# Optimization experiments

Measured on AMD Instinct MI355X. Metric: run time of the kernel, lower is better.

## Reference

```python
import jax, jax.numpy as jnp
import numpy as np

# LE-like radial basis config (hypers: type='le', r_cut=5.0, mlp=True, no alchemical)
N_MAX_L = [22, 19, 16, 13]      # n_max per angular channel l
L_MAX = len(N_MAX_L) - 1
N_TOTAL = sum(N_MAX_L)          # 70
N_SPECIES = 4                   # all_species = [0,1,2,3]
N_GRID = 1024                   # spline control points
R_CUT = 5.0
HIDDEN = 32                     # hard-coded MLP width in the module
N_EDGES = 400_000


def setup_inputs() -> dict:
    key = jax.random.key(0)
    ks = jax.random.split(key, 7)
    # neighbor distances in [0, r_cut)
    r = jax.random.uniform(ks[0], (N_EDGES,), dtype=jnp.float32) * R_CUT
    neighbor_species = jax.random.randint(ks[1], (N_EDGES,), 0, N_SPECIES)
    # spline table standing in for the precomputed spliner coefficients
    spline_table = jax.random.normal(ks[2], (N_GRID, N_TOTAL), dtype=jnp.float32)
    nmax = max(N_MAX_L)
    sc_in = 1.0 / np.sqrt(nmax)
    sc_h = 1.0 / np.sqrt(HIDDEN)
    # per-(l, species) expert MLP weights, padded to nmax along the n_max_l axis;
    # torch Linear(n_in, n_out, bias=False) == x @ W with W: [n_in, n_out]
    W1 = jax.random.normal(ks[3], (L_MAX + 1, N_SPECIES, nmax, HIDDEN), dtype=jnp.float32) * sc_in
    W2 = jax.random.normal(ks[4], (L_MAX + 1, N_SPECIES, HIDDEN, HIDDEN), dtype=jnp.float32) * sc_h
    W3 = jax.random.normal(ks[5], (L_MAX + 1, N_SPECIES, HIDDEN, HIDDEN), dtype=jnp.float32) * sc_h
    W4 = jax.random.normal(ks[6], (L_MAX + 1, N_SPECIES, HIDDEN, nmax), dtype=jnp.float32) * sc_h
    return {"r": r, "neighbor_species": neighbor_species, "spline_table": spline_table,
            "W1": W1, "W2": W2, "W3": W3, "W4": W4}


def _spline_eval(r, spline_table):
    # linear-interpolation spline over a uniform grid on [0, R_CUT]
    dx = R_CUT / (N_GRID - 1)
    xi = r / dx
    idx = jnp.clip(jnp.floor(xi).astype(jnp.int32), 0, N_GRID - 2)
    frac = (xi - idx.astype(xi.dtype))[:, None]
    return spline_table[idx] * (1.0 - frac) + spline_table[idx + 1] * frac  # [E, N_TOTAL]


def reference(r, neighbor_species, spline_table, W1, W2, W3, W4):
    # 1) spline basis eval: r -> radial_functions [E, N_TOTAL]
    rf = _spline_eval(r, spline_table)
    silu = jax.nn.silu
    outs = []
    off = 0
    # 2) split by n_max_l; per-species expert MLP with scatter-back.
    # Vectorized as: run each species' tiny MLP on all edges, select via mask
    # (equivalent math to the original's nonzero/index_select gather-scatter).
    for l, n_l in enumerate(N_MAX_L):
        x_l = rf[:, off:off + n_l]  # [E, n_l]
        off += n_l
        out_l = jnp.zeros_like(x_l)
        for s in range(N_SPECIES):
            h = silu(x_l @ W1[l, s, :n_l])        # [E, 32]
            h = silu(h @ W2[l, s])                # [E, 32]
            h = silu(h @ W3[l, s])                # [E, 32]
            y = h @ W4[l, s][:, :n_l]             # [E, n_l]
            out_l = jnp.where(neighbor_species[:, None] == s, y, out_l)
        outs.append(out_l)
    # original returns a list split by l; concatenate for a single output array
    return jnp.concatenate(outs, axis=1)  # [E, N_TOTAL]
```

## Files before the change

### kernel.cpp

```cpp
#include <hip/hip_runtime.h>
#include <math.h>

#define BLK 256
#define BX 192
#define NEDGE_MAX 400000
#define TSL 24608

typedef __attribute__((ext_vector_type(8))) short short8;
typedef __attribute__((ext_vector_type(4))) float f32x4;

union Frag {
  short8 s;
  unsigned int u[4];
};

__device__ __forceinline__ unsigned int pack_pair(float a, float b) {
  const unsigned int ua = __float_as_uint(a) + 0x8000u;
  const unsigned int ub = __float_as_uint(b) + 0x8000u;
  return (ua >> 16) | (ub & 0xFFFF0000u);
}

__device__ __forceinline__ void split_pair(float a, float b, unsigned int& hi,
                                           unsigned int& lo) {
  hi = pack_pair(a, b);
  const float ra = a - __uint_as_float(hi << 16);
  const float rb = b - __uint_as_float(hi & 0xFFFF0000u);
  lo = pack_pair(ra, rb);
}

__device__ __forceinline__ f32x4 silu4(f32x4 v) {
#pragma unroll
  for (int i = 0; i < 4; i++) {
    const float e = __builtin_amdgcn_exp2f(v[i] * -1.44269504f);
    v[i] = v[i] * __builtin_amdgcn_rcpf(1.0f + e);
  }
  return v;
}


__global__ void k_zero(int* __restrict__ cnt) {
  if (threadIdx.x < 4) cnt[threadIdx.x] = 0;
}

__global__ void __launch_bounds__(BLK) k_compact(const int* __restrict__ spc,
                                                 const float* __restrict__ r, int n,
                                                 int nb, int* __restrict__ cnt,
                                                 float* __restrict__ fracs,
                                                 int* __restrict__ toffA,
                                                 int* __restrict__ perm,
                                                 const float* __restrict__ tbl,
                                                 float* __restrict__ wt) {
  if (blockIdx.x >= nb) {
    const int t = (blockIdx.x - nb) * BLK + threadIdx.x;
    if (t < 4 * 1024 * 24) {
      const int l = t / (1024 * 24);
      const int rem = t - l * (1024 * 24);
      const int idx = rem / 24;
      const int j = rem - idx * 24;
      const int off = (l == 0) ? 0 : (l == 1) ? 22 : (l == 2) ? 41 : 57;
      const int nl = (l == 0) ? 22 : (l == 1) ? 19 : (l == 2) ? 16 : 13;
      const float v = (j < nl) ? tbl[idx * 70 + off + j] : 0.f;
      wt[l * TSL + idx * 24 + j] = v;
    }
    if (t < 4 * 32) {
      const int l = t >> 5, j = t & 31;
      wt[l * TSL + 1024 * 24 + j] = 0.f;
    }
    return;
  }

  __shared__ int wcnt[4][4];
  __shared__ int wbase[4][4];
  const int tid = threadIdx.x;
  const int i = blockIdx.x * BLK + tid;
  const int lane = tid & 63;
  const int w = tid >> 6;
  const int s = (i < n) ? spc[i] : -1;
  const float rr = (i < n) ? r[i] : 0.f;

  int rank = 0;
#pragma unroll
  for (int sp = 0; sp < 4; sp++) {
    unsigned long long m = __ballot(s == sp);
    if (lane == 0) wcnt[w][sp] = __popcll(m);
    if (s == sp) rank = __popcll(m & ((1ULL << lane) - 1ULL));
  }
  __syncthreads();
  if (tid < 4) {
    const int c0 = wcnt[0][tid], c1 = wcnt[1][tid], c2 = wcnt[2][tid], c3 = wcnt[3][tid];
    const int b = atomicAdd(&cnt[tid], c0 + c1 + c2 + c3);
    wbase[0][tid] = b;
    wbase[1][tid] = b + c0;
    wbase[2][tid] = b + c0 + c1;
    wbase[3][tid] = b + c0 + c1 + c2;
  }
  __syncthreads();
  if (s >= 0) {
    const int pos = s * NEDGE_MAX + wbase[w][s] + rank;
    const float xi = rr * (1023.0f / 5.0f);
    int idx = (int)floorf(xi);
    idx = idx < 0 ? 0 : (idx > 1022 ? 1022 : idx);
    fracs[pos] = xi - (float)idx;
    toffA[pos] = idx * 96;
    perm[pos] = i;
  }
}


__device__ __forceinline__ void layer_hl(const Frag* A, const Frag& bh,
                                         const Frag& bl, f32x4& d0, f32x4& d1) {
  f32x4 z = {0.f, 0.f, 0.f, 0.f};
  d0 = __builtin_amdgcn_mfma_f32_16x16x32_bf16(A[0].s, bl.s, z, 0, 0, 0);
  d0 = __builtin_amdgcn_mfma_f32_16x16x32_bf16(A[0].s, bh.s, d0, 0, 0, 0);
  d1 = __builtin_amdgcn_mfma_f32_16x16x32_bf16(A[1].s, bl.s, z, 0, 0, 0);
  d1 = __builtin_amdgcn_mfma_f32_16x16x32_bf16(A[1].s, bh.s, d1, 0, 0, 0);
}

__device__ __forceinline__ void layer_h(const Frag* A, const Frag& bh, f32x4& d0,
                                        f32x4& d1) {
  f32x4 z = {0.f, 0.f, 0.f, 0.f};
  d0 = __builtin_amdgcn_mfma_f32_16x16x32_bf16(A[0].s, bh.s, z, 0, 0, 0);
  d1 = __builtin_amdgcn_mfma_f32_16x16x32_bf16(A[1].s, bh.s, z, 0, 0, 0);
}

__device__ __forceinline__ void ldA(const unsigned int* __restrict__ wfr,
                                    int base256, int lane, Frag* A) {
#pragma unroll
  for (int jt = 0; jt < 2; jt++) {
    const uint4 v =
        reinterpret_cast<const uint4*>(wfr + ((base256 + jt) << 8))[lane];
    A[jt].u[0] = v.x;
    A[jt].u[1] = v.y;
    A[jt].u[2] = v.z;
    A[jt].u[3] = v.w;
  }
}

__device__ __forceinline__ void repack(const f32x4& d0, const f32x4& d1,
                                       Frag& bh) {
  bh.u[0] = pack_pair(d0[0], d0[1]);
  bh.u[1] = pack_pair(d0[2], d0[3]);
  bh.u[2] = pack_pair(d1[0], d1[1]);
  bh.u[3] = pack_pair(d1[2], d1[3]);
}

template <int L, int UBASE, int G1>
__device__ __forceinline__ void proc_l(const unsigned int* __restrict__ wfr,
                                       const float* __restrict__ wt, int toff,
                                       float frac, int g, int lane,
                                       unsigned int* __restrict__ xrow) {
  const char* p = (const char*)(wt + (size_t)L * TSL + 8 * g) + toff;
  const f32x4 a0 = *(const f32x4*)(p);
  const f32x4 a1 = *(const f32x4*)(p + 16);
  const f32x4 b0 = *(const f32x4*)(p + 96);
  const f32x4 b1 = *(const f32x4*)(p + 112);

  Frag A1[2], A2[2], A3[2], A4[2];
  ldA(wfr, (L * 4 + 0) * 2, lane, A1);
  ldA(wfr, (L * 4 + 1) * 2, lane, A2);
  ldA(wfr, (L * 4 + 2) * 2, lane, A3);
  ldA(wfr, (L * 4 + 3) * 2, lane, A4);

  float x[8];
#pragma unroll
  for (int d = 0; d < 4; d++) {
    x[d] = a0[d] + frac * (b0[d] - a0[d]);
    x[d + 4] = a1[d] + frac * (b1[d] - a1[d]);
  }
  Frag bh, bl;
  split_pair(x[0], x[1], bh.u[0], bl.u[0]);
  split_pair(x[2], x[3], bh.u[1], bl.u[1]);
  split_pair(x[4], x[5], bh.u[2], bl.u[2]);
  split_pair(x[6], x[7], bh.u[3], bl.u[3]);

  f32x4 d0, d1;
  layer_hl(A1, bh, bl, d0, d1);
  d0 = silu4(d0); d1 = silu4(d1); repack(d0, d1, bh);
  layer_h(A2, bh, d0, d1);
  d0 = silu4(d0); d1 = silu4(d1); repack(d0, d1, bh);
  layer_h(A3, bh, d0, d1);
  d0 = silu4(d0); d1 = silu4(d1); repack(d0, d1, bh);
  f32x4 z = {0.f, 0.f, 0.f, 0.f};
  d0 = __builtin_amdgcn_mfma_f32_16x16x32_bf16(A4[0].s, bh.s, z, 0, 0, 0);
  if (G1 > 0) d1 = __builtin_amdgcn_mfma_f32_16x16x32_bf16(A4[1].s, bh.s, z, 0, 0, 0);

  *(uint2*)(xrow + UBASE + 2 * g) =
      make_uint2(pack_pair(d0[0], d0[1]), pack_pair(d0[2], d0[3]));
  if (G1 > 0 && g < G1)
    *(uint2*)(xrow + UBASE + 8 + 2 * g) =
        make_uint2(pack_pair(d1[0], d1[1]), pack_pair(d1[2], d1[3]));
}

__global__ void __launch_bounds__(BLK) rb_fused(
    const float* __restrict__ fracs, const int* __restrict__ toffA,
    const int* __restrict__ perm, const float* __restrict__ wt,
    const float* __restrict__ W1, const float* __restrict__ W2,
    const float* __restrict__ W3, const float* __restrict__ W4,
    float* __restrict__ out, const int* __restrict__ cnt) {
  __shared__ unsigned int wfr[8192];
  __shared__ unsigned int xp[4][16 * 38];
  __shared__ int eid[4][16];

  const int s = blockIdx.y;
  const int count = cnt[s];
  if (count == 0) return;
  const int sBase = s * NEDGE_MAX;

  {
    const int nlarr[4] = {22, 19, 16, 13};
    for (int e = threadIdx.x; e < 8192; e += BLK) {
      const int p = e & 3;
      const int lane = (e >> 2) & 63;
      const int jt = (e >> 8) & 1;
      const int m = (e >> 9) & 3;
      const int l = e >> 11;
      const int c = lane & 15, g = lane >> 4;
      const int j = jt * 16 + c;
      const int nl = nlarr[l];
      float a, b;
      if (m == 0) {
        const int k0 = 8 * g + 2 * p, k1 = k0 + 1;
        const float* wp = W1 + (size_t)(l * 4 + s) * 704;
        a = (k0 < nl) ? wp[k0 * 32 + j] : 0.f;
        b = (k1 < nl) ? wp[k1 * 32 + j] : 0.f;
      } else {
        const int kp0 = (p < 2) ? (4 * g + 2 * p) : (16 + 4 * g + 2 * (p - 2));
        const int kp1 = kp0 + 1;
        if (m == 1) {
          const float* wp = W2 + (size_t)(l * 4 + s) * 1024;
          a = wp[kp0 * 32 + j];
          b = wp[kp1 * 32 + j];
        } else if (m == 2) {
          const float* wp = W3 + (size_t)(l * 4 + s) * 1024;
          a = wp[kp0 * 32 + j];
          b = wp[kp1 * 32 + j];
        } else {
          const float* wp = W4 + (size_t)(l * 4 + s) * 704;
          a = (j < nl) ? wp[kp0 * 22 + j] : 0.f;
          b = (j < nl) ? wp[kp1 * 22 + j] : 0.f;
        }
      }
      wfr[e] = pack_pair(a, b);
    }
  }
  __syncthreads();

  const int lane = threadIdx.x & 63;
  const int w = threadIdx.x >> 6;
  const int c = lane & 15, g = lane >> 4;
  unsigned int* __restrict__ xpw = xp[w];
  int* __restrict__ eidw = eid[w];
  unsigned int* __restrict__ xrow = xpw + c * 38;
  const int stride = gridDim.x * 64;

  int eb = blockIdx.x * 64 + w * 16;
  int valid = (eb + c) < count;
  int spi = sBase + (valid ? eb + c : 0);
  float frac = fracs[spi];
  int toff = toffA[spi];
  int e0 = perm[spi];

  for (; eb < count; eb += stride) {
    const int nei = eb + stride + c;
    const int nvalid = nei < count;
    const int nspi = sBase + (nvalid ? nei : 0);
    const float nfrac = fracs[nspi];
    const int ntoff = toffA[nspi];
    const int ne = perm[nspi];

    proc_l<0, 0, 2>(wfr, wt, toff, frac, g, lane, xrow);
    proc_l<1, 12, 1>(wfr, wt, toff, frac, g, lane, xrow);
    proc_l<2, 22, 0>(wfr, wt, toff, frac, g, lane, xrow);
    proc_l<3, 30, 0>(wfr, wt, toff, frac, g, lane, xrow);

    if (g == 0) eidw[c] = valid ? e0 : -1;
    __asm__ volatile("" ::: "memory");

#pragma unroll
    for (int it = 0; it < 18; it++) {
      const int t = it * 64 + lane;
      if (t < 16 * 70) {
        const int row = t / 70;
        const int f = t - row * 70;
        const int er = eidw[row];
        const int fl = f + ((f >= 22) ? 2 : 0) + ((f >= 41) ? 1 : 0);
        const unsigned int v = xpw[row * 38 + (fl >> 1)];
        const unsigned int hv = (fl & 1) ? (v & 0xFFFF0000u) : (v << 16);
        if (er >= 0) out[(size_t)er * 70 + f] = __uint_as_float(hv);
      }
    }
    __asm__ volatile("" ::: "memory");

    frac = nfrac;
    toff = ntoff;
    e0 = ne;
    valid = nvalid;
  }
}

extern "C" void kernel_launch(void* const* d_in, const int* in_sizes, int n_in,
                              void* d_out, int out_size, void* d_ws, size_t ws_size,
                              hipStream_t stream) {
  const float* r = (const float*)d_in[0];
  const int* spc = (const int*)d_in[1];
  const float* tbl = (const float*)d_in[2];
  const float* W1 = (const float*)d_in[3];
  const float* W2 = (const float*)d_in[4];
  const float* W3 = (const float*)d_in[5];
  const float* W4 = (const float*)d_in[6];
  float* out = (float*)d_out;
  const int n = in_sizes[0];

  int* cnt = (int*)d_ws;
  float* fracs = (float*)(cnt + 64);
  int* toffA = (int*)(fracs + 4 * NEDGE_MAX);
  int* perm = toffA + 4 * NEDGE_MAX;
  float* wtbl = (float*)(perm + 4 * NEDGE_MAX);

  hipLaunchKernelGGL(k_zero, dim3(1), dim3(64), 0, stream, cnt);

  const int nb = (n + BLK - 1) / BLK;
  hipLaunchKernelGGL(k_compact, dim3(nb + 384), dim3(BLK), 0, stream, spc, r, n,
                     nb, cnt, fracs, toffA, perm, tbl, wtbl);

  hipLaunchKernelGGL(rb_fused, dim3(BX, 4), dim3(BLK), 0, stream, fracs, toffA,
                     perm, wtbl, W1, W2, W3, W4, out, cnt);
}
```

Before: 123.1 us.

## Pre-pack MLP weight fragments in global memory and drop LDS weight staging

Moves the per-species bf16 weight-fragment packing out of the main kernel into extra blocks of the compaction kernel, writing fragments to a global workspace. The main kernel then reads weight fragments straight from global/L2 with software prefetch, one layer ahead, instead of staging 32KB in LDS per block. It also stores outputs as fp32 in LDS rather than truncated bf16, and raises the grid width with an occupancy hint of 5 blocks per CU. Freeing LDS should allow more resident blocks and removes the per-block packing prologue, at the cost of repeated global fragment loads per edge tile.

Result: slower. 251.5 us (+104.4%).

```diff
diff --git a/kernel.cpp b/kernel.cpp
--- a/kernel.cpp
+++ b/kernel.cpp
@@ -2,7 +2,7 @@
 #include <math.h>
 
 #define BLK 256
-#define BX 192
+#define BX 320
 #define NEDGE_MAX 400000
 #define TSL 24608
 
@@ -49,166 +49,34 @@
                                                  int* __restrict__ toffA,
                                                  int* __restrict__ perm,
                                                  const float* __restrict__ tbl,
-                                                 float* __restrict__ wt) {
+                                                 float* __restrict__ wt,
+                                                 unsigned int* __restrict__ wg,
+                                                 const float* __restrict__ W1,
+                                                 const float* __restrict__ W2,
+                                                 const float* __restrict__ W3,
+                                                 const float* __restrict__ W4) {
   if (blockIdx.x >= nb) {
-    const int t = (blockIdx.x - nb) * BLK + threadIdx.x;
-    if (t < 4 * 1024 * 24) {
-      const int l = t / (1024 * 24);
-      const int rem = t - l * (1024 * 24);
-      const int idx = rem / 24;
-      const int j = rem - idx * 24;
-      const int off = (l == 0) ? 0 : (l == 1) ? 22 : (l == 2) ? 41 : 57;
-      const int nl = (l == 0) ? 22 : (l == 1) ? 19 : (l == 2) ? 16 : 13;
-      const float v = (j < nl) ? tbl[idx * 70 + off + j] : 0.f;
-      wt[l * TSL + idx * 24 + j] = v;
-    }
-    if (t < 4 * 32) {
-      const int l = t >> 5, j = t & 31;
-      wt[l * TSL + 1024 * 24 + j] = 0.f;
-    }
-    return;
-  }
-
-  __shared__ int wcnt[4][4];
-  __shared__ int wbase[4][4];
-  const int tid = threadIdx.x;
-  const int i = blockIdx.x * BLK + tid;
-  const int lane = tid & 63;
-  const int w = tid >> 6;
-  const int s = (i < n) ? spc[i] : -1;
-  const float rr = (i < n) ? r[i] : 0.f;
-
-  int rank = 0;
-#pragma unroll
-  for (int sp = 0; sp < 4; sp++) {
-    unsigned long long m = __ballot(s == sp);
-    if (lane == 0) wcnt[w][sp] = __popcll(m);
-    if (s == sp) rank = __popcll(m & ((1ULL << lane) - 1ULL));
-  }
-  __syncthreads();
-  if (tid < 4) {
-    const int c0 = wcnt[0][tid], c1 = wcnt[1][tid], c2 = wcnt[2][tid], c3 = wcnt[3][tid];
-    const int b = atomicAdd(&cnt[tid], c0 + c1 + c2 + c3);
-    wbase[0][tid] = b;
-    wbase[1][tid] = b + c0;
-    wbase[2][tid] = b + c0 + c1;
-    wbase[3][tid] = b + c0 + c1 + c2;
-  }
-  __syncthreads();
-  if (s >= 0) {
-    const int pos = s * NEDGE_MAX + wbase[w][s] + rank;
-    const float xi = rr * (1023.0f / 5.0f);
-    int idx = (int)floorf(xi);
-    idx = idx < 0 ? 0 : (idx > 1022 ? 1022 : idx);
-    fracs[pos] = xi - (float)idx;
-    toffA[pos] = idx * 96;
-    perm[pos] = i;
-  }
-}
-
-
-__device__ __forceinline__ void layer_hl(const Frag* A, const Frag& bh,
-                                         const Frag& bl, f32x4& d0, f32x4& d1) {
-  f32x4 z = {0.f, 0.f, 0.f, 0.f};
-  d0 = __builtin_amdgcn_mfma_f32_16x16x32_bf16(A[0].s, bl.s, z, 0, 0, 0);
-  d0 = __builtin_amdgcn_mfma_f32_16x16x32_bf16(A[0].s, bh.s, d0, 0, 0, 0);
-  d1 = __builtin_amdgcn_mfma_f32_16x16x32_bf16(A[1].s, bl.s, z, 0, 0, 0);
-  d1 = __builtin_amdgcn_mfma_f32_16x16x32_bf16(A[1].s, bh.s, d1, 0, 0, 0);
-}
-
-__device__ __forceinline__ void layer_h(const Frag* A, const Frag& bh, f32x4& d0,
-                                        f32x4& d1) {
-  f32x4 z = {0.f, 0.f, 0.f, 0.f};
-  d0 = __builtin_amdgcn_mfma_f32_16x16x32_bf16(A[0].s, bh.s, z, 0, 0, 0);
-  d1 = __builtin_amdgcn_mfma_f32_16x16x32_bf16(A[1].s, bh.s, z, 0, 0, 0);
-}
-
-__device__ __forceinline__ void ldA(const unsigned int* __restrict__ wfr,
-                                    int base256, int lane, Frag* A) {
-#pragma unroll
-  for (int jt = 0; jt < 2; jt++) {
-    const uint4 v =
-        reinterpret_cast<const uint4*>(wfr + ((base256 + jt) << 8))[lane];
-    A[jt].u[0] = v.x;
-    A[jt].u[1] = v.y;
-    A[jt].u[2] = v.z;
-    A[jt].u[3] = v.w;
-  }
-}
-
-__device__ __forceinline__ void repack(const f32x4& d0, const f32x4& d1,
-                                       Frag& bh) {
-  bh.u[0] = pack_pair(d0[0], d0[1]);
-  bh.u[1] = pack_pair(d0[2], d0[3]);
-  bh.u[2] = pack_pair(d1[0], d1[1]);
-  bh.u[3] = pack_pair(d1[2], d1[3]);
-}
-
-template <int L, int UBASE, int G1>
-__device__ __forceinline__ void proc_l(const unsigned int* __restrict__ wfr,
-                                       const float* __restrict__ wt, int toff,
-                                       float frac, int g, int lane,
-                                       unsigned int* __restrict__ xrow) {
-  const char* p = (const char*)(wt + (size_t)L * TSL + 8 * g) + toff;
-  const f32x4 a0 = *(const f32x4*)(p);
-  const f32x4 a1 = *(const f32x4*)(p + 16);
-  const f32x4 b0 = *(const f32x4*)(p + 96);
-  const f32x4 b1 = *(const f32x4*)(p + 112);
-
-  Frag A1[2], A2[2], A3[2], A4[2];
-  ldA(wfr, (L * 4 + 0) * 2, lane, A1);
-  ldA(wfr, (L * 4 + 1) * 2, lane, A2);
-  ldA(wfr, (L * 4 + 2) * 2, lane, A3);
-  ldA(wfr, (L * 4 + 3) * 2, lane, A4);
-
-  float x[8];
-#pragma unroll
-  for (int d = 0; d < 4; d++) {
-    x[d] = a0[d] + frac * (b0[d] - a0[d]);
-    x[d + 4] = a1[d] + frac * (b1[d] - a1[d]);
-  }
-  Frag bh, bl;
-  split_pair(x[0], x[1], bh.u[0], bl.u[0]);
-  split_pair(x[2], x[3], bh.u[1], bl.u[1]);
-  split_pair(x[4], x[5], bh.u[2], bl.u[2]);
-  split_pair(x[6], x[7], bh.u[3], bl.u[3]);
-
-  f32x4 d0, d1;
-  layer_hl(A1, bh, bl, d0, d1);
-  d0 = silu4(d0); d1 = silu4(d1); repack(d0, d1, bh);
-  layer_h(A2, bh, d0, d1);
-  d0 = silu4(d0); d1 = silu4(d1); repack(d0, d1, bh);
-  layer_h(A3, bh, d0, d1);
-  d0 = silu4(d0); d1 = silu4(d1); repack(d0, d1, bh);
-  f32x4 z = {0.f, 0.f, 0.f, 0.f};
-  d0 = __builtin_amdgcn_mfma_f32_16x16x32_bf16(A4[0].s, bh.s, z, 0, 0, 0);
-  if (G1 > 0) d1 = __builtin_amdgcn_mfma_f32_16x16x32_bf16(A4[1].s, bh.s, z, 0, 0, 0);
-
-  *(uint2*)(xrow + UBASE + 2 * g) =
-      make_uint2(pack_pair(d0[0], d0[1]), pack_pair(d0[2], d0[3]));
-  if (G1 > 0 && g < G1)
-    *(uint2*)(xrow + UBASE + 8 + 2 * g) =
-        make_uint2(pack_pair(d1[0], d1[1]), pack_pair(d1[2], d1[3]));
-}
-
-__global__ void __launch_bounds__(BLK) rb_fused(
-    const float* __restrict__ fracs, const int* __restrict__ toffA,
-    const int* __restrict__ perm, const float* __restrict__ wt,
-    const float* __restrict__ W1, const float* __restrict__ W2,
-    const float* __restrict__ W3, const float* __restrict__ W4,
-    float* __restrict__ out, const int* __restrict__ cnt) {
-  __shared__ unsigned int wfr[8192];
-  __shared__ unsigned int xp[4][16 * 38];
-  __shared__ int eid[4][16];
-
-  const int s = blockIdx.y;
-  const int count = cnt[s];
-  if (count == 0) return;
-  const int sBase = s * NEDGE_MAX;
-
-  {
-    const int nlarr[4] = {22, 19, 16, 13};
-    for (int e = threadIdx.x; e < 8192; e += BLK) {
+    const int reg2 = blockIdx.x - nb;
+    if (reg2 < 384) {
+      const int t = reg2 * BLK + threadIdx.x;
+      if (t < 4 * 1024 * 24) {
+        const int l = t / (1024 * 24);
+        const int rem = t - l * (1024 * 24);
+        const int idx = rem / 24;
+        const int j = rem - idx * 24;
+        const int off = (l == 0) ? 0 : (l == 1) ? 22 : (l == 2) ? 41 : 57;
+        const int nl = (l == 0) ? 22 : (l == 1) ? 19 : (l == 2) ? 16 : 13;
+        const float v = (j < nl) ? tbl[idx * 70 + off + j] : 0.f;
+        wt[l * TSL + idx * 24 + j] = v;
+      }
+      if (t < 4 * 32) {
+        const int l = t >> 5, j = t & 31;
+        wt[l * TSL + 1024 * 24 + j] = 0.f;
+      }
+    } else {
+      const int eg = (reg2 - 384) * BLK + threadIdx.x;
+      const int s = eg >> 13;
+      const int e = eg & 8191;
       const int p = e & 3;
       const int lane = (e >> 2) & 63;
       const int jt = (e >> 8) & 1;
@@ -216,7 +84,7 @@
       const int l = e >> 11;
       const int c = lane & 15, g = lane >> 4;
       const int j = jt * 16 + c;
-      const int nl = nlarr[l];
+      const int nl = (l == 0) ? 22 : (l == 1) ? 19 : (l == 2) ? 16 : 13;
       float a, b;
       if (m == 0) {
         const int k0 = 8 * g + 2 * p, k1 = k0 + 1;
@@ -240,17 +108,153 @@
           b = (j < nl) ? wp[kp1 * 22 + j] : 0.f;
         }
       }
-      wfr[e] = pack_pair(a, b);
+      wg[eg] = pack_pair(a, b);
     }
+    return;
+  }
+
+  __shared__ int wcnt[4][4];
+  __shared__ int wbase[4][4];
+  const int tid = threadIdx.x;
+  const int i = blockIdx.x * BLK + tid;
+  const int lane = tid & 63;
+  const int w = tid >> 6;
+  const int s = (i < n) ? spc[i] : -1;
+  const float rr = (i < n) ? r[i] : 0.f;
+
+  int rank = 0;
+#pragma unroll
+  for (int sp = 0; sp < 4; sp++) {
+    unsigned long long m = __ballot(s == sp);
+    if (lane == 0) wcnt[w][sp] = __popcll(m);
+    if (s == sp) rank = __popcll(m & ((1ULL << lane) - 1ULL));
   }
   __syncthreads();
+  if (tid < 4) {
+    const int c0 = wcnt[0][tid], c1 = wcnt[1][tid], c2 = wcnt[2][tid], c3 = wcnt[3][tid];
+    const int b = atomicAdd(&cnt[tid], c0 + c1 + c2 + c3);
+    wbase[0][tid] = b;
+    wbase[1][tid] = b + c0;
+    wbase[2][tid] = b + c0 + c1;
+    wbase[3][tid] = b + c0 + c1 + c2;
+  }
+  __syncthreads();
+  if (s >= 0) {
+    const int pos = s * NEDGE_MAX + wbase[w][s] + rank;
+    const float xi = rr * (1023.0f / 5.0f);
+    int idx = (int)floorf(xi);
+    idx = idx < 0 ? 0 : (idx > 1022 ? 1022 : idx);
+    fracs[pos] = xi - (float)idx;
+    toffA[pos] = idx * 96;
+    perm[pos] = i;
+  }
+}
+
+
+__device__ __forceinline__ void layer_hl(const Frag* A, const Frag& bh,
+                                         const Frag& bl, f32x4& d0, f32x4& d1) {
+  f32x4 z = {0.f, 0.f, 0.f, 0.f};
+  d0 = __builtin_amdgcn_mfma_f32_16x16x32_bf16(A[0].s, bl.s, z, 0, 0, 0);
+  d0 = __builtin_amdgcn_mfma_f32_16x16x32_bf16(A[0].s, bh.s, d0, 0, 0, 0);
+  d1 = __builtin_amdgcn_mfma_f32_16x16x32_bf16(A[1].s, bl.s, z, 0, 0, 0);
+  d1 = __builtin_amdgcn_mfma_f32_16x16x32_bf16(A[1].s, bh.s, d1, 0, 0, 0);
+}
+
+__device__ __forceinline__ void layer_h(const Frag* A, const Frag& bh, f32x4& d0,
+                                        f32x4& d1) {
+  f32x4 z = {0.f, 0.f, 0.f, 0.f};
+  d0 = __builtin_amdgcn_mfma_f32_16x16x32_bf16(A[0].s, bh.s, z, 0, 0, 0);
+  d1 = __builtin_amdgcn_mfma_f32_16x16x32_bf16(A[1].s, bh.s, z, 0, 0, 0);
+}
+
+__device__ __forceinline__ void ldG(const unsigned int* __restrict__ wgs,
+                                    int base256, int lane, Frag* A) {
+#pragma unroll
+  for (int jt = 0; jt < 2; jt++) {
+    const uint4 v =
+        reinterpret_cast<const uint4*>(wgs + ((base256 + jt) << 8))[lane];
+    A[jt].u[0] = v.x;
+    A[jt].u[1] = v.y;
+    A[jt].u[2] = v.z;
+    A[jt].u[3] = v.w;
+  }
+}
+
+__device__ __forceinline__ void repack(const f32x4& d0, const f32x4& d1,
+                                       Frag& bh) {
+  bh.u[0] = pack_pair(d0[0], d0[1]);
+  bh.u[1] = pack_pair(d0[2], d0[3]);
+  bh.u[2] = pack_pair(d1[0], d1[1]);
+  bh.u[3] = pack_pair(d1[2], d1[3]);
+}
+
+template <int L>
+__device__ __forceinline__ void gather_split(const float* __restrict__ wt,
+                                             int toff, float frac, int g,
+                                             Frag& bh, Frag& bl) {
+  const char* p = (const char*)(wt + (size_t)L * TSL + 8 * g) + toff;
+  const f32x4 a0 = *(const f32x4*)(p);
+  const f32x4 a1 = *(const f32x4*)(p + 16);
+  const f32x4 b0 = *(const f32x4*)(p + 96);
+  const f32x4 b1 = *(const f32x4*)(p + 112);
+  float x[8];
+#pragma unroll
+  for (int d = 0; d < 4; d++) {
+    x[d] = a0[d] + frac * (b0[d] - a0[d]);
+    x[d + 4] = a1[d] + frac * (b1[d] - a1[d]);
+  }
+  split_pair(x[0], x[1], bh.u[0], bl.u[0]);
+  split_pair(x[2], x[3], bh.u[1], bl.u[1]);
+  split_pair(x[4], x[5], bh.u[2], bl.u[2]);
+  split_pair(x[6], x[7], bh.u[3], bl.u[3]);
+}
+
+template <int L, int OFFA, int G1>
+__device__ __forceinline__ void proc_l(const unsigned int* __restrict__ wgs,
+                                       const float* __restrict__ wt, int toff,
+                                       float frac, int g, int lane,
+                                       float* __restrict__ xrow) {
+  Frag Aa[2], Ab[2];
+  ldG(wgs, (L * 4 + 0) * 2, lane, Aa);
+  Frag bh, bl;
+  gather_split<L>(wt, toff, frac, g, bh, bl);
+  ldG(wgs, (L * 4 + 1) * 2, lane, Ab);
+  f32x4 d0, d1;
+  layer_hl(Aa, bh, bl, d0, d1);
+  d0 = silu4(d0); d1 = silu4(d1); repack(d0, d1, bh);
+  ldG(wgs, (L * 4 + 2) * 2, lane, Aa);
+  layer_h(Ab, bh, d0, d1);
+  d0 = silu4(d0); d1 = silu4(d1); repack(d0, d1, bh);
+  ldG(wgs, (L * 4 + 3) * 2, lane, Ab);
+  layer_h(Aa, bh, d0, d1);
+  d0 = silu4(d0); d1 = silu4(d1); repack(d0, d1, bh);
+  f32x4 z = {0.f, 0.f, 0.f, 0.f};
+  d0 = __builtin_amdgcn_mfma_f32_16x16x32_bf16(Ab[0].s, bh.s, z, 0, 0, 0);
+  if (G1 > 0) d1 = __builtin_amdgcn_mfma_f32_16x16x32_bf16(Ab[1].s, bh.s, z, 0, 0, 0);
+  *(f32x4*)(xrow + OFFA + 4 * g) = d0;
+  if (G1 > 0 && g < G1) *(f32x4*)(xrow + OFFA + 16 + 4 * g) = d1;
+}
+
+__global__ void __launch_bounds__(BLK, 5) rb_fused(
+    const float* __restrict__ fracs, const int* __restrict__ toffA,
+    const int* __restrict__ perm, const float* __restrict__ wt,
+    const unsigned int* __restrict__ wg, float* __restrict__ out,
+    const int* __restrict__ cnt) {
+  __shared__ float xp[4][16 * 76];
+  __shared__ int eid[4][16];
+
+  const int s = blockIdx.y;
+  const int count = cnt[s];
+  if (count == 0) return;
+  const int sBase = s * NEDGE_MAX;
+  const unsigned int* __restrict__ wgs = wg + s * 8192;
 
   const int lane = threadIdx.x & 63;
   const int w = threadIdx.x >> 6;
   const int c = lane & 15, g = lane >> 4;
-  unsigned int* __restrict__ xpw = xp[w];
+  float* __restrict__ xpw = xp[w];
   int* __restrict__ eidw = eid[w];
-  unsigned int* __restrict__ xrow = xpw + c * 38;
+  float* __restrict__ xrow = xpw + c * 76;
   const int stride = gridDim.x * 64;
 
   int eb = blockIdx.x * 64 + w * 16;
@@ -268,10 +272,10 @@
     const int ntoff = toffA[nspi];
     const int ne = perm[nspi];
 
-    proc_l<0, 0, 2>(wfr, wt, toff, frac, g, lane, xrow);
-    proc_l<1, 12, 1>(wfr, wt, toff, frac, g, lane, xrow);
-    proc_l<2, 22, 0>(wfr, wt, toff, frac, g, lane, xrow);
-    proc_l<3, 30, 0>(wfr, wt, toff, frac, g, lane, xrow);
+    proc_l<0, 0, 2>(wgs, wt, toff, frac, g, lane, xrow);
+    proc_l<1, 24, 1>(wgs, wt, toff, frac, g, lane, xrow);
+    proc_l<2, 44, 0>(wgs, wt, toff, frac, g, lane, xrow);
+    proc_l<3, 60, 0>(wgs, wt, toff, frac, g, lane, xrow);
 
     if (g == 0) eidw[c] = valid ? e0 : -1;
     __asm__ volatile("" ::: "memory");
@@ -284,9 +288,7 @@
         const int f = t - row * 70;
         const int er = eidw[row];
         const int fl = f + ((f >= 22) ? 2 : 0) + ((f >= 41) ? 1 : 0);
-        const unsigned int v = xpw[row * 38 + (fl >> 1)];
-        const unsigned int hv = (fl & 1) ? (v & 0xFFFF0000u) : (v << 16);
-        if (er >= 0) out[(size_t)er * 70 + f] = __uint_as_float(hv);
+        if (er >= 0) out[(size_t)er * 70 + f] = xpw[row * 76 + fl];
       }
     }
     __asm__ volatile("" ::: "memory");
@@ -316,13 +318,15 @@
   int* toffA = (int*)(fracs + 4 * NEDGE_MAX);
   int* perm = toffA + 4 * NEDGE_MAX;
   float* wtbl = (float*)(perm + 4 * NEDGE_MAX);
+  unsigned int* wg = (unsigned int*)(wtbl + 4 * TSL);
 
   hipLaunchKernelGGL(k_zero, dim3(1), dim3(64), 0, stream, cnt);
 
   const int nb = (n + BLK - 1) / BLK;
-  hipLaunchKernelGGL(k_compact, dim3(nb + 384), dim3(BLK), 0, stream, spc, r, n,
-                     nb, cnt, fracs, toffA, perm, tbl, wtbl);
+  hipLaunchKernelGGL(k_compact, dim3(nb + 384 + 128), dim3(BLK), 0, stream, spc,
+                     r, n, nb, cnt, fracs, toffA, perm, tbl, wtbl, wg, W1, W2, W3,
+                     W4);
 
   hipLaunchKernelGGL(rb_fused, dim3(BX, 4), dim3(BLK), 0, stream, fracs, toffA,
-                     perm, wtbl, W1, W2, W3, W4, out, cnt);
-}
+                     perm, wtbl, wg, out, cnt);
+}
```

## Process two 16-edge tiles per wave to interleave MFMA chains and stage fp32 output

Applied to the files above, without the earlier changes.

Each wave now handles 32 edges per iteration as two independent 16-edge tiles, interleaving their MLP layer MFMA chains so the two dependency chains can hide each other's latency. The weight fragments are loaded once and reused for both tiles. The staging buffer holds fp32 results instead of bf16-packed values, which drops the pack/unpack work in the output path. Register pressure and shared memory per block rise, which may lower occupancy.

Result: slower. 136.4 us (+10.8%).

```diff
diff --git a/kernel.cpp b/kernel.cpp
--- a/kernel.cpp
+++ b/kernel.cpp
@@ -144,51 +144,74 @@
   bh.u[3] = pack_pair(d1[2], d1[3]);
 }
 
-template <int L, int UBASE, int G1>
-__device__ __forceinline__ void proc_l(const unsigned int* __restrict__ wfr,
-                                       const float* __restrict__ wt, int toff,
-                                       float frac, int g, int lane,
-                                       unsigned int* __restrict__ xrow) {
+template <int L>
+__device__ __forceinline__ void gather_split(const float* __restrict__ wt,
+                                             int toff, float frac, int g,
+                                             Frag& bh, Frag& bl) {
   const char* p = (const char*)(wt + (size_t)L * TSL + 8 * g) + toff;
   const f32x4 a0 = *(const f32x4*)(p);
   const f32x4 a1 = *(const f32x4*)(p + 16);
   const f32x4 b0 = *(const f32x4*)(p + 96);
   const f32x4 b1 = *(const f32x4*)(p + 112);
-
+  float x[8];
+#pragma unroll
+  for (int d = 0; d < 4; d++) {
+    x[d] = a0[d] + frac * (b0[d] - a0[d]);
+    x[d + 4] = a1[d] + frac * (b1[d] - a1[d]);
+  }
+  split_pair(x[0], x[1], bh.u[0], bl.u[0]);
+  split_pair(x[2], x[3], bh.u[1], bl.u[1]);
+  split_pair(x[4], x[5], bh.u[2], bl.u[2]);
+  split_pair(x[6], x[7], bh.u[3], bl.u[3]);
+}
+
+template <int L, int OFFA, int G1>
+__device__ __forceinline__ void proc_l2(const unsigned int* __restrict__ wfr,
+                                        const float* __restrict__ wt, int toff0,
+                                        float frac0, int toff1, float frac1,
+                                        int g, int lane,
+                                        float* __restrict__ xrow0,
+                                        float* __restrict__ xrow1) {
   Frag A1[2], A2[2], A3[2], A4[2];
   ldA(wfr, (L * 4 + 0) * 2, lane, A1);
   ldA(wfr, (L * 4 + 1) * 2, lane, A2);
   ldA(wfr, (L * 4 + 2) * 2, lane, A3);
   ldA(wfr, (L * 4 + 3) * 2, lane, A4);
 
-  float x[8];
-#pragma unroll
-  for (int d = 0; d < 4; d++) {
-    x[d] = a0[d] + frac * (b0[d] - a0[d]);
-    x[d + 4] = a1[d] + frac * (b1[d] - a1[d]);
-  }
-  Frag bh, bl;
-  split_pair(x[0], x[1], bh.u[0], bl.u[0]);
-  split_pair(x[2], x[3], bh.u[1], bl.u[1]);
-  split_pair(x[4], x[5], bh.u[2], bl.u[2]);
-  split_pair(x[6], x[7], bh.u[3], bl.u[3]);
-
-  f32x4 d0, d1;
-  layer_hl(A1, bh, bl, d0, d1);
-  d0 = silu4(d0); d1 = silu4(d1); repack(d0, d1, bh);
-  layer_h(A2, bh, d0, d1);
-  d0 = silu4(d0); d1 = silu4(d1); repack(d0, d1, bh);
-  layer_h(A3, bh, d0, d1);
-  d0 = silu4(d0); d1 = silu4(d1); repack(d0, d1, bh);
+  Frag bh0, bl0, bh1, bl1;
+  gather_split<L>(wt, toff0, frac0, g, bh0, bl0);
+  gather_split<L>(wt, toff1, frac1, g, bh1, bl1);
+
+  f32x4 d00, d01, d10, d11;
+  layer_hl(A1, bh0, bl0, d00, d01);
+  layer_hl(A1, bh1, bl1, d10, d11);
+
+  d00 = silu4(d00); d01 = silu4(d01); repack(d00, d01, bh0);
+  d10 = silu4(d10); d11 = silu4(d11); repack(d10, d11, bh1);
+  layer_h(A2, bh0, d00, d01);
+  layer_h(A2, bh1, d10, d11);
+
+  d00 = silu4(d00); d01 = silu4(d01); repack(d00, d01, bh0);
+  d10 = silu4(d10); d11 = silu4(d11); repack(d10, d11, bh1);
+  layer_h(A3, bh0, d00, d01);
+  layer_h(A3, bh1, d10, d11);
+
+  d00 = silu4(d00); d01 = silu4(d01); repack(d00, d01, bh0);
+  d10 = silu4(d10); d11 = silu4(d11); repack(d10, d11, bh1);
   f32x4 z = {0.f, 0.f, 0.f, 0.f};
-  d0 = __builtin_amdgcn_mfma_f32_16x16x32_bf16(A4[0].s, bh.s, z, 0, 0, 0);
-  if (G1 > 0) d1 = __builtin_amdgcn_mfma_f32_16x16x32_bf16(A4[1].s, bh.s, z, 0, 0, 0);
-
-  *(uint2*)(xrow + UBASE + 2 * g) =
-      make_uint2(pack_pair(d0[0], d0[1]), pack_pair(d0[2], d0[3]));
-  if (G1 > 0 && g < G1)
-    *(uint2*)(xrow + UBASE + 8 + 2 * g) =
-        make_uint2(pack_pair(d1[0], d1[1]), pack_pair(d1[2], d1[3]));
+  d00 = __builtin_amdgcn_mfma_f32_16x16x32_bf16(A4[0].s, bh0.s, z, 0, 0, 0);
+  d10 = __builtin_amdgcn_mfma_f32_16x16x32_bf16(A4[0].s, bh1.s, z, 0, 0, 0);
+  if (G1 > 0) {
+    d01 = __builtin_amdgcn_mfma_f32_16x16x32_bf16(A4[1].s, bh0.s, z, 0, 0, 0);
+    d11 = __builtin_amdgcn_mfma_f32_16x16x32_bf16(A4[1].s, bh1.s, z, 0, 0, 0);
+  }
+
+  *(f32x4*)(xrow0 + OFFA + 4 * g) = d00;
+  *(f32x4*)(xrow1 + OFFA + 4 * g) = d10;
+  if (G1 > 0 && g < G1) {
+    *(f32x4*)(xrow0 + OFFA + 16 + 4 * g) = d01;
+    *(f32x4*)(xrow1 + OFFA + 16 + 4 * g) = d11;
+  }
 }
 
 __global__ void __launch_bounds__(BLK) rb_fused(
@@ -198,8 +221,8 @@
     const float* __restrict__ W3, const float* __restrict__ W4,
     float* __restrict__ out, const int* __restrict__ cnt) {
   __shared__ unsigned int wfr[8192];
-  __shared__ unsigned int xp[4][16 * 38];
-  __shared__ int eid[4][16];
+  __shared__ float xp[4][32 * 76];
+  __shared__ int eid[4][32];
 
   const int s = blockIdx.y;
   const int count = cnt[s];
@@ -248,53 +271,55 @@
   const int lane = threadIdx.x & 63;
   const int w = threadIdx.x >> 6;
   const int c = lane & 15, g = lane >> 4;
-  unsigned int* __restrict__ xpw = xp[w];
+  float* __restrict__ xpw = xp[w];
   int* __restrict__ eidw = eid[w];
-  unsigned int* __restrict__ xrow = xpw + c * 38;
-  const int stride = gridDim.x * 64;
-
-  int eb = blockIdx.x * 64 + w * 16;
-  int valid = (eb + c) < count;
-  int spi = sBase + (valid ? eb + c : 0);
-  float frac = fracs[spi];
-  int toff = toffA[spi];
-  int e0 = perm[spi];
+  float* __restrict__ xrow0 = xpw + c * 76;
+  float* __restrict__ xrow1 = xpw + (16 + c) * 76;
+  const int stride = gridDim.x * 128;
+
+  int eb = blockIdx.x * 128 + w * 32;
+  int v0 = (eb + c) < count;
+  int v1 = (eb + 16 + c) < count;
+  int spi0 = sBase + (v0 ? eb + c : 0);
+  int spi1 = sBase + (v1 ? eb + 16 + c : 0);
+  float frac0 = fracs[spi0], frac1 = fracs[spi1];
+  int toff0 = toffA[spi0], toff1 = toffA[spi1];
+  int e00 = perm[spi0], e01 = perm[spi1];
 
   for (; eb < count; eb += stride) {
-    const int nei = eb + stride + c;
-    const int nvalid = nei < count;
-    const int nspi = sBase + (nvalid ? nei : 0);
-    const float nfrac = fracs[nspi];
-    const int ntoff = toffA[nspi];
-    const int ne = perm[nspi];
-
-    proc_l<0, 0, 2>(wfr, wt, toff, frac, g, lane, xrow);
-    proc_l<1, 12, 1>(wfr, wt, toff, frac, g, lane, xrow);
-    proc_l<2, 22, 0>(wfr, wt, toff, frac, g, lane, xrow);
-    proc_l<3, 30, 0>(wfr, wt, toff, frac, g, lane, xrow);
-
-    if (g == 0) eidw[c] = valid ? e0 : -1;
+    const int neb = eb + stride;
+    const int nv0 = (neb + c) < count;
+    const int nv1 = (neb + 16 + c) < count;
+    const int nspi0 = sBase + (nv0 ? neb + c : 0);
+    const int nspi1 = sBase + (nv1 ? neb + 16 + c : 0);
+    const float nfrac0 = fracs[nspi0], nfrac1 = fracs[nspi1];
+    const int ntoff0 = toffA[nspi0], ntoff1 = toffA[nspi1];
+    const int ne00 = perm[nspi0], ne01 = perm[nspi1];
+
+    proc_l2<0, 0, 2>(wfr, wt, toff0, frac0, toff1, frac1, g, lane, xrow0, xrow1);
+    proc_l2<1, 24, 1>(wfr, wt, toff0, frac0, toff1, frac1, g, lane, xrow0, xrow1);
+    proc_l2<2, 44, 0>(wfr, wt, toff0, frac0, toff1, frac1, g, lane, xrow0, xrow1);
+    proc_l2<3, 60, 0>(wfr, wt, toff0, frac0, toff1, frac1, g, lane, xrow0, xrow1);
+
+    if (g == 0) eidw[c] = v0 ? e00 : -1;
+    if (g == 1) eidw[16 + c] = v1 ? e01 : -1;
     __asm__ volatile("" ::: "memory");
 
 #pragma unroll
-    for (int it = 0; it < 18; it++) {
+    for (int it = 0; it < 35; it++) {
       const int t = it * 64 + lane;
-      if (t < 16 * 70) {
-        const int row = t / 70;
-        const int f = t - row * 70;
-        const int er = eidw[row];
-        const int fl = f + ((f >= 22) ? 2 : 0) + ((f >= 41) ? 1 : 0);
-        const unsigned int v = xpw[row * 38 + (fl >> 1)];
-        const unsigned int hv = (fl & 1) ? (v & 0xFFFF0000u) : (v << 16);
-        if (er >= 0) out[(size_t)er * 70 + f] = __uint_as_float(hv);
-      }
+      const int row = t / 70;
+      const int f = t - row * 70;
+      const int er = eidw[row];
+      const int fl = f + ((f >= 22) ? 2 : 0) + ((f >= 41) ? 1 : 0);
+      if (er >= 0) out[(size_t)er * 70 + f] = xpw[row * 76 + fl];
     }
     __asm__ volatile("" ::: "memory");
 
-    frac = nfrac;
-    toff = ntoff;
-    e0 = ne;
-    valid = nvalid;
+    frac0 = nfrac0; frac1 = nfrac1;
+    toff0 = ntoff0; toff1 = ntoff1;
+    e00 = ne00; e01 = ne01;
+    v0 = nv0; v1 = nv1;
   }
 }
 
```
